# Optimization experiments

Hardware: AMD Instinct MI355X
Metric: run time of the kernel (lower is better)

Reference implementation:

```python
import jax, jax.numpy as jnp
import numpy as np

DIM, HEADS, RANK = 768, 12, 64
HEAD_DIM = DIM // HEADS

def _xavier(key, shape):
    fan_in, fan_out = shape[1], shape[0]
    std = (2.0 / (fan_in + fan_out)) ** 0.5
    return std * jax.random.normal(key, shape, dtype=jnp.float32)

def setup_inputs() -> dict:
    key = jax.random.key(0)
    ks = jax.random.split(key, 12)
    B, N = 8, 1024
    x = jax.random.normal(ks[0], (B, N, DIM), dtype=jnp.float32)
    params = {}
    for i, nm in enumerate(['Q', 'K', 'V']):
        params[f'W_{nm}0'] = _xavier(ks[1 + 3 * i], (DIM, RANK))
        params[f'W_{nm}1'] = _xavier(ks[2 + 3 * i], (HEADS, RANK))
        params[f'W_{nm}2'] = _xavier(ks[3 + 3 * i], (HEAD_DIM, RANK))
    proj_w = _xavier(ks[10], (DIM, DIM))
    proj_b = jnp.zeros((DIM,), dtype=jnp.float32)
    return dict(x=x, W_Q0=params['W_Q0'], W_Q1=params['W_Q1'], W_Q2=params['W_Q2'],
                W_K0=params['W_K0'], W_K1=params['W_K1'], W_K2=params['W_K2'],
                W_V0=params['W_V0'], W_V1=params['W_V1'], W_V2=params['W_V2'],
                proj_w=proj_w, proj_b=proj_b)

def _cp_proj(xh, W2, W1, W0, B, N, H, hd):
    # xh: [B,N,H,hd]; contract head_dim with W2 and heads with W1 -> [B,N,R], then expand to dim via W0
    t = jnp.einsum('blnd,dr,nr->blr', xh, W2, W1)
    out = jnp.einsum('blr,mr->blm', t, W0)          # [B,N,dim]
    return out.reshape(B, N, H, hd).transpose(0, 2, 1, 3)  # [B,H,N,hd]

def reference(x, W_Q0, W_Q1, W_Q2, W_K0, W_K1, W_K2, W_V0, W_V1, W_V2, proj_w, proj_b):
    B, N, C = x.shape
    H = W_Q1.shape[0]
    hd = C // H
    scale = hd ** -0.5
    xh = x.reshape(B, N, H, hd)
    q = _cp_proj(xh, W_Q2, W_Q1, W_Q0, B, N, H, hd)
    k = _cp_proj(xh, W_K2, W_K1, W_K0, B, N, H, hd)
    v = _cp_proj(xh, W_V2, W_V1, W_V0, B, N, H, hd)
    attn = jax.nn.softmax(jnp.einsum('bhqd,bhkd->bhqk', q, k) * scale, axis=-1)
    out = jnp.einsum('bhqk,bhkd->bhqd', attn, v).transpose(0, 2, 1, 3).reshape(B, N, C)
    return out @ proj_w.T + proj_b
```

## Files before the change

kernel.cpp:

```cpp
#include <hip/hip_runtime.h>

typedef unsigned short u16;
typedef __attribute__((ext_vector_type(8))) short bf16x8;
typedef __attribute__((ext_vector_type(4))) float f32x4;
typedef __attribute__((ext_vector_type(4))) unsigned short u16x4;
typedef __attribute__((ext_vector_type(8))) unsigned short u16x8;

#define AS1 __attribute__((address_space(1)))
#define AS3 __attribute__((address_space(3)))

__device__ __forceinline__ float b2f(u16 s) {
    return __uint_as_float(((unsigned)s) << 16);
}
__device__ __forceinline__ u16 f2b(float f) {
    unsigned u = __float_as_uint(f);
    unsigned r = 0x7fffu + ((u >> 16) & 1u);
    return (u16)((u + r) >> 16);
}

__device__ __forceinline__ unsigned packtrunc(float p0, float p1) {
#if __has_builtin(__builtin_amdgcn_perm)
    return __builtin_amdgcn_perm(__float_as_uint(p1), __float_as_uint(p0), 0x07060302u);
#else
    return (__float_as_uint(p0) >> 16) | (__float_as_uint(p1) & 0xffff0000u);
#endif
}

__device__ __forceinline__ void g2l16(const u16* g, u16* l) {
    __builtin_amdgcn_global_load_lds((const AS1 void*)g, (AS3 void*)l, 16, 0, 0);
}

#if __has_builtin(__builtin_amdgcn_exp2f)
#define EXP2(x) __builtin_amdgcn_exp2f(x)
#else
#define EXP2(x) exp2f(x)
#endif

__global__ __launch_bounds__(256) void build_prep(
    const float* __restrict__ Wq0, const float* __restrict__ Wq1, const float* __restrict__ Wq2,
    const float* __restrict__ Wk0, const float* __restrict__ Wk1, const float* __restrict__ Wk2,
    const float* __restrict__ Wv0, const float* __restrict__ Wv1, const float* __restrict__ Wv2,
    const float* __restrict__ PW,
    u16* __restrict__ G, u16* __restrict__ MqkT, u16* __restrict__ Dcat)
{
    const int bx = blockIdx.x;
    const int t = threadIdx.x;
    if (bx < 576) {
        const int idx = bx * 256 + t;
        const int row = idx / 768, c = idx - row * 768;
        const int which = row >> 6, r = row & 63;
        const int h = c >> 6, d = c & 63;
        const float* W1 = (which == 0) ? Wq1 : (which == 1) ? Wk1 : Wv1;
        const float* W2 = (which == 0) ? Wq2 : (which == 1) ? Wk2 : Wv2;
        G[idx] = f2b(W1[h * 64 + r] * W2[d * 64 + r]);
    } else if (bx < 624) {
        __shared__ float wq[64 * 65];
        __shared__ float wk[64 * 65];
        const int hq = bx - 576;
        const int h = hq >> 2, quarter = hq & 3;
        const float qs = 0.125f * 1.4426950408889634f;
        for (int i = t; i < 4096; i += 256) {
            const int dd = i >> 6, r = i & 63;
            wq[dd * 65 + r] = Wq0[(h * 64 + dd) * 64 + r] * qs;
            wk[dd * 65 + r] = Wk0[(h * 64 + dd) * 64 + r];
        }
        __syncthreads();
        const int j0 = quarter * 1024 + t * 4;
        const int r2 = j0 >> 6, r1b = j0 & 63;
        u16x4 pk;
#pragma unroll
        for (int jj = 0; jj < 4; ++jj) {
            float acc = 0.f;
#pragma unroll
            for (int dd = 0; dd < 64; ++dd)
                acc += wk[dd * 65 + r2] * wq[dd * 65 + r1b + jj];
            ((u16*)&pk)[jj] = f2b(acc);
        }
        *(u16x4*)(MqkT + (size_t)(h * 64 + r2) * 64 + r1b) = pk;
    } else {
        __shared__ float w0s[64 * 65];
        __shared__ float pws[32 * 65];
        const int hb = bx - 624;
        const int h = hb / 24, mBase = (hb - h * 24) * 32;
        for (int i = t; i < 4096; i += 256) {
            const int d = i >> 6, r = i & 63;
            w0s[d * 65 + r] = Wv0[(h * 64 + d) * 64 + r];
        }
        for (int i = t; i < 2048; i += 256) {
            const int mi = i >> 6, d = i & 63;
            pws[mi * 65 + d] = PW[(size_t)(mBase + mi) * 768 + h * 64 + d];
        }
        __syncthreads();
        const int r = t & 63, mi0 = t >> 6;
        float w0c[64];
#pragma unroll
        for (int d = 0; d < 64; ++d) w0c[d] = w0s[d * 65 + r];
        for (int mi = mi0; mi < 32; mi += 4) {
            float acc = 0.f;
#pragma unroll
            for (int d = 0; d < 64; ++d) acc += pws[mi * 65 + d] * w0c[d];
            Dcat[(size_t)(mBase + mi) * 768 + h * 64 + r] = f2b(acc);
        }
    }
}

__global__ __launch_bounds__(256, 2) void gemm_t(
    const float* __restrict__ X, const u16* __restrict__ G,
    u16* __restrict__ T, u16* __restrict__ tvt)
{
    __shared__ u16 As[64 * 32];
    __shared__ u16 Bs[64 * 32];

    const int tid = threadIdx.x;
    const int lane = tid & 63, wv = tid >> 6;
    const int l15 = lane & 15, quad = lane >> 4;

    const int lin = blockIdx.x + 3 * blockIdx.y;
    const int xcd = lin & 7, j = lin >> 3;
    const int col = j % 3, rowhi = j / 3;
    const int rowBase = (rowhi * 8 + xcd) * 64;
    const int colBase = col * 64;

    const int srow = tid >> 2;
    const int scol = (tid & 3) * 8;
    const float* aS = X + (size_t)(rowBase + srow) * 768 + scol;
    const u16*  bS  = G + (size_t)(colBase + srow) * 768 + scol;

    float4 a0 = *(const float4*)(aS);
    float4 a1 = *(const float4*)(aS + 4);
    int4   b0 = *(const int4*)(bS);

    const f32x4 zero4 = {0.f, 0.f, 0.f, 0.f};
    f32x4 acc[4];
#pragma unroll
    for (int tn = 0; tn < 4; ++tn) acc[tn] = zero4;

    for (int kk = 0; kk < 768; kk += 32) {
        __syncthreads();
        u16x8 ap;
        ap[0] = f2b(a0.x); ap[1] = f2b(a0.y); ap[2] = f2b(a0.z); ap[3] = f2b(a0.w);
        ap[4] = f2b(a1.x); ap[5] = f2b(a1.y); ap[6] = f2b(a1.z); ap[7] = f2b(a1.w);
        *(u16x8*)&As[srow * 32 + scol] = ap;
        *(int4*)&Bs[srow * 32 + scol]  = b0;
        __syncthreads();

        if (kk < 736) {
            a0 = *(const float4*)(aS + kk + 32);
            a1 = *(const float4*)(aS + kk + 36);
            b0 = *(const int4*)(bS + kk + 32);
        }

        const bf16x8 af = *(const bf16x8*)(As + (wv * 16 + l15) * 32 + quad * 8);
#pragma unroll
        for (int tn = 0; tn < 4; ++tn) {
            const bf16x8 bf = *(const bf16x8*)(Bs + (tn * 16 + l15) * 32 + quad * 8);
            acc[tn] = __builtin_amdgcn_mfma_f32_16x16x32_bf16(af, bf, acc[tn], 0, 0, 0);
        }
    }

    if (colBase < 128) {
#pragma unroll
        for (int tn = 0; tn < 4; ++tn) {
            const int c = colBase + tn * 16 + l15;
#pragma unroll
            for (int r = 0; r < 4; ++r) {
                const int grow = rowBase + wv * 16 + quad * 4 + r;
                T[(size_t)grow * 128 + c] = f2b(acc[tn][r]);
            }
        }
    } else {
#pragma unroll
        for (int tn = 0; tn < 4; ++tn) {
            const int rr = tn * 16 + l15;
            const int grow = rowBase + wv * 16 + quad * 4;
            u16x4 pk;
            pk.x = f2b(acc[tn][0]); pk.y = f2b(acc[tn][1]);
            pk.z = f2b(acc[tn][2]); pk.w = f2b(acc[tn][3]);
            *(u16x4*)(tvt + (size_t)rr * 8192 + grow) = pk;
        }
    }
}

__global__ __launch_bounds__(256, 3) void flash_attn10(
    const u16* __restrict__ T, const u16* __restrict__ MqkT,
    const u16* __restrict__ tvt, u16* __restrict__ Z)
{
    const int bh = blockIdx.x;
    const int qt = blockIdx.y;
    const int b = bh / 12, h = bh - b * 12;
    const u16* qp = T + ((size_t)b * 1024 + qt * 128) * 128;
    const u16* kp = T + (size_t)b * 1024 * 128 + 64;
    const u16* vp = tvt + b * 1024;

    __shared__ u16 B0raw[2 * 64 * 72];
    __shared__ u16 B1raw[2 * 64 * 72];

    const int t = threadIdx.x;
    const int lane = t & 63, wv = t >> 6;
    const int l15 = lane & 15, quad = lane >> 4;

    bf16x8 qf[2][2];
#pragma unroll
    for (int qg = 0; qg < 2; ++qg) {
        const u16* qrow = qp + (size_t)(wv * 32 + qg * 16 + l15) * 128;
        qf[qg][0] = *(const bf16x8*)(qrow + quad * 8);
        qf[qg][1] = *(const bf16x8*)(qrow + 32 + quad * 8);
    }

    const int srow = t >> 2;
    const int scol = (t & 3) * 16;
    const int p5 = srow & 31;
    const int lrow = (srow & 32) | ((p5 & 4) << 2) | ((p5 & 16) >> 1)
                   | ((p5 & 8) >> 1) | (p5 & 3);

    bf16x8 vone = {};
    if (l15 == 0) {
#pragma unroll
        for (int j = 0; j < 8; ++j) vone[j] = (short)0x3F80;
    }

    int4 kr0 = *(const int4*)(kp + (size_t)srow * 128 + scol);
    int4 kr1 = *(const int4*)(kp + (size_t)srow * 128 + scol + 8);
    int4 vr0 = *(const int4*)(vp + (size_t)srow * 8192 + scol);
    int4 vr1 = *(const int4*)(vp + (size_t)srow * 8192 + scol + 8);

    const f32x4 zero4 = {0.f, 0.f, 0.f, 0.f};
    {
        f32x4 Wt[2][4];
#pragma unroll
        for (int qg = 0; qg < 2; ++qg)
#pragma unroll
            for (int tn = 0; tn < 4; ++tn) Wt[qg][tn] = zero4;
#pragma unroll
        for (int ks = 0; ks < 2; ++ks) {
#pragma unroll
            for (int tn = 0; tn < 4; ++tn) {
                const bf16x8 mb = *(const bf16x8*)(
                    MqkT + (size_t)(h * 64 + tn * 16 + l15) * 64 + ks * 32 + quad * 8);
                Wt[0][tn] = __builtin_amdgcn_mfma_f32_16x16x32_bf16(qf[0][ks], mb, Wt[0][tn], 0, 0, 0);
                Wt[1][tn] = __builtin_amdgcn_mfma_f32_16x16x32_bf16(qf[1][ks], mb, Wt[1][tn], 0, 0, 0);
            }
        }
#pragma unroll
        for (int qg = 0; qg < 2; ++qg)
#pragma unroll
            for (int tn = 0; tn < 4; ++tn)
#pragma unroll
                for (int r = 0; r < 4; ++r)
                    B1raw[(wv * 32 + qg * 16 + quad * 4 + r) * 72 + tn * 16 + l15] =
                        f2b(Wt[qg][tn][r]);
    }
    __syncthreads();
    bf16x8 wf[2][2];
#pragma unroll
    for (int qg = 0; qg < 2; ++qg) {
        wf[qg][0] = *(const bf16x8*)&B1raw[(wv * 32 + qg * 16 + l15) * 72 + quad * 8];
        wf[qg][1] = *(const bf16x8*)&B1raw[(wv * 32 + qg * 16 + l15) * 72 + 32 + quad * 8];
    }

    *(int4*)&B0raw[lrow * 72 + scol]                 = kr0;
    *(int4*)&B0raw[lrow * 72 + scol + 8]             = kr1;
    *(int4*)&B0raw[64 * 72 + srow * 72 + scol]       = vr0;
    *(int4*)&B0raw[64 * 72 + srow * 72 + scol + 8]   = vr1;
    kr0 = *(const int4*)(kp + (size_t)(64 + srow) * 128 + scol);
    kr1 = *(const int4*)(kp + (size_t)(64 + srow) * 128 + scol + 8);
    vr0 = *(const int4*)(vp + (size_t)srow * 8192 + 64 + scol);
    vr1 = *(const int4*)(vp + (size_t)srow * 8192 + 64 + scol + 8);
    __syncthreads();

    f32x4 o_acc[2][4];
    f32x4 Lacc[2] = {zero4, zero4};
#pragma unroll
    for (int qg = 0; qg < 2; ++qg)
#pragma unroll
        for (int tn = 0; tn < 4; ++tn) o_acc[qg][tn] = zero4;

#define STAGE(NB)                                                               \
    {                                                                           \
        *(int4*)&NB[lrow * 72 + scol]               = kr0;                      \
        *(int4*)&NB[lrow * 72 + scol + 8]           = kr1;                      \
        *(int4*)&NB[64 * 72 + srow * 72 + scol]     = vr0;                      \
        *(int4*)&NB[64 * 72 + srow * 72 + scol + 8] = vr1;                      \
    }
#define PREFETCH(KT)                                                            \
    {                                                                           \
        kr0 = *(const int4*)(kp + (size_t)((KT) * 64 + srow) * 128 + scol);     \
        kr1 = *(const int4*)(kp + (size_t)((KT) * 64 + srow) * 128 + scol + 8); \
        vr0 = *(const int4*)(vp + (size_t)srow * 8192 + (KT) * 64 + scol);      \
        vr1 = *(const int4*)(vp + (size_t)srow * 8192 + (KT) * 64 + scol + 8);  \
    }
#define FLASH_TILE(KB)                                                          \
    {                                                                           \
        f32x4 Sacc[2][4];                                                       \
        _Pragma("unroll")                                                       \
        for (int qg = 0; qg < 2; ++qg)                                          \
            _Pragma("unroll")                                                   \
            for (int tk = 0; tk < 4; ++tk) Sacc[qg][tk] = zero4;                \
        _Pragma("unroll")                                                       \
        for (int ks = 0; ks < 2; ++ks) {                                        \
            _Pragma("unroll")                                                   \
            for (int tk = 0; tk < 4; ++tk) {                                    \
                const bf16x8 kf = *(const bf16x8*)&KB[(tk * 16 + l15) * 72 + ks * 32 + quad * 8]; \
                Sacc[0][tk] = __builtin_amdgcn_mfma_f32_16x16x32_bf16(kf, wf[0][ks], Sacc[0][tk], 0, 0, 0); \
                Sacc[1][tk] = __builtin_amdgcn_mfma_f32_16x16x32_bf16(kf, wf[1][ks], Sacc[1][tk], 0, 0, 0); \
            }                                                                   \
        }                                                                       \
        union { bf16x8 v; unsigned u[4]; } pf[2][2];                            \
        _Pragma("unroll")                                                       \
        for (int qg = 0; qg < 2; ++qg)                                          \
            _Pragma("unroll")                                                   \
            for (int tk = 0; tk < 4; ++tk) {                                    \
                const float p0 = EXP2(Sacc[qg][tk][0]);                         \
                const float p1 = EXP2(Sacc[qg][tk][1]);                         \
                const float p2 = EXP2(Sacc[qg][tk][2]);                         \
                const float p3 = EXP2(Sacc[qg][tk][3]);                         \
                const int g = tk >> 1, hf = (tk & 1) * 2;                       \
                pf[qg][g].u[hf + 0] = packtrunc(p0, p1);                        \
                pf[qg][g].u[hf + 1] = packtrunc(p2, p3);                        \
            }                                                                   \
        _Pragma("unroll")                                                       \
        for (int g = 0; g < 2; ++g) {                                           \
            _Pragma("unroll")                                                   \
            for (int tn = 0; tn < 4; ++tn) {                                    \
                const bf16x8 vf = *(const bf16x8*)&KB[64 * 72 + (tn * 16 + l15) * 72 + g * 32 + quad * 8]; \
                o_acc[0][tn] = __builtin_amdgcn_mfma_f32_16x16x32_bf16(pf[0][g].v, vf, o_acc[0][tn], 0, 0, 0); \
                o_acc[1][tn] = __builtin_amdgcn_mfma_f32_16x16x32_bf16(pf[1][g].v, vf, o_acc[1][tn], 0, 0, 0); \
            }                                                                   \
            Lacc[0] = __builtin_amdgcn_mfma_f32_16x16x32_bf16(pf[0][g].v, vone, Lacc[0], 0, 0, 0); \
            Lacc[1] = __builtin_amdgcn_mfma_f32_16x16x32_bf16(pf[1][g].v, vone, Lacc[1], 0, 0, 0); \
        }                                                                       \
    }

    for (int t8 = 0; t8 < 8; ++t8) {
        const int kt0 = 2 * t8;
        STAGE(B1raw);
        if (t8 < 7) PREFETCH(kt0 + 2);
        FLASH_TILE(B0raw);
        __syncthreads();
        if (t8 < 7) {
            STAGE(B0raw);
            PREFETCH(kt0 + 3);
        }
        FLASH_TILE(B1raw);
        if (t8 < 7) __syncthreads();
    }

#undef STAGE
#undef PREFETCH
#undef FLASH_TILE

#pragma unroll
    for (int qg = 0; qg < 2; ++qg) {
#pragma unroll
        for (int r = 0; r < 4; ++r) {
            const float Lv = __shfl(Lacc[qg][r], quad << 4, 64);
            const float inv = 1.0f / Lv;
            const int token = qt * 128 + wv * 32 + qg * 16 + quad * 4 + r;
#pragma unroll
            for (int tn = 0; tn < 4; ++tn) {
                const int col = h * 64 + tn * 16 + l15;
                Z[(size_t)(b * 1024 + token) * 768 + col] = f2b(o_acc[qg][tn][r] * inv);
            }
        }
    }
}

__global__ __launch_bounds__(256, 3) void gemm_out(
    const u16* __restrict__ A, const u16* __restrict__ Bt,
    float* __restrict__ C, const float* __restrict__ bias)
{
    __shared__ u16 As[128 * 32];
    __shared__ u16 Bs[64 * 32];

    const int tid  = threadIdx.x;
    const int lane = tid & 63, wv = tid >> 6;
    const int l15  = lane & 15, quad = lane >> 4;

    const int lin = blockIdx.x + 12 * blockIdx.y;
    const int xcd = lin & 7, j = lin >> 3;
    const int colT = j % 12, rowhi = j / 12;
    const int rowBase = (rowhi * 8 + xcd) * 128;
    const int colBase = colT * 64;

    const int srowA = wv * 32 + (lane >> 2);
    const int srowB = wv * 16 + (lane >> 2);
    const int scol  = (lane & 3) * 8;
    const u16* aSrc = A  + (size_t)(rowBase + srowA) * 768 + scol;
    const u16* bSrc = Bt + (size_t)(colBase + srowB) * 768 + scol;
    u16* aDst = As + wv * 1024;
    u16* bDst = Bs + wv * 512;

    const f32x4 zero4 = {0.f, 0.f, 0.f, 0.f};
    f32x4 acc[2][4];
#pragma unroll
    for (int tm = 0; tm < 2; ++tm)
#pragma unroll
        for (int tn = 0; tn < 4; ++tn) acc[tm][tn] = zero4;

    for (int kk = 0; kk < 768; kk += 32) {
        __syncthreads();
        g2l16(aSrc + kk,            aDst);
        g2l16(aSrc + kk + 16 * 768, aDst + 512);
        g2l16(bSrc + kk,            bDst);
        __syncthreads();

        bf16x8 af[2], bfm[4];
#pragma unroll
        for (int t = 0; t < 2; ++t)
            af[t]  = *(const bf16x8*)(As + (wv * 32 + t * 16 + l15) * 32 + quad * 8);
#pragma unroll
        for (int t = 0; t < 4; ++t)
            bfm[t] = *(const bf16x8*)(Bs + (t * 16 + l15) * 32 + quad * 8);
#pragma unroll
        for (int tm = 0; tm < 2; ++tm)
#pragma unroll
            for (int tn = 0; tn < 4; ++tn)
                acc[tm][tn] = __builtin_amdgcn_mfma_f32_16x16x32_bf16(
                    af[tm], bfm[tn], acc[tm][tn], 0, 0, 0);
    }

#pragma unroll
    for (int tm = 0; tm < 2; ++tm) {
        const int grow = rowBase + wv * 32 + tm * 16 + quad * 4;
#pragma unroll
        for (int tn = 0; tn < 4; ++tn) {
            const int gcol = colBase + tn * 16 + l15;
            const float bv = bias[gcol];
#pragma unroll
            for (int r = 0; r < 4; ++r)
                C[(size_t)(grow + r) * 768 + gcol] = acc[tm][tn][r] + bv;
        }
    }
}

extern "C" void kernel_launch(void* const* d_in, const int* in_sizes, int n_in,
                              void* d_out, int out_size, void* d_ws, size_t ws_size,
                              hipStream_t stream)
{
    const float* x      = (const float*)d_in[0];
    const float* Wq0    = (const float*)d_in[1];
    const float* Wq1    = (const float*)d_in[2];
    const float* Wq2    = (const float*)d_in[3];
    const float* Wk0    = (const float*)d_in[4];
    const float* Wk1    = (const float*)d_in[5];
    const float* Wk2    = (const float*)d_in[6];
    const float* Wv0    = (const float*)d_in[7];
    const float* Wv1    = (const float*)d_in[8];
    const float* Wv2    = (const float*)d_in[9];
    const float* proj_w = (const float*)d_in[10];
    const float* proj_b = (const float*)d_in[11];
    float* outp = (float*)d_out;

    char* ws = (char*)d_ws;
    u16* T    = (u16*)ws;
    u16* tvt  = (u16*)(ws + 2097152);
    u16* G    = (u16*)(ws + 3145728);
    u16* MqkT = (u16*)(ws + 3440640);
    u16* Dcat = (u16*)(ws + 3538944);
    u16* Zcat = (u16*)(ws + 4718592);

    build_prep<<<912, 256, 0, stream>>>(Wq0, Wq1, Wq2, Wk0, Wk1, Wk2, Wv0, Wv1, Wv2,
                                        proj_w, G, MqkT, Dcat);
    gemm_t<<<dim3(3, 128), 256, 0, stream>>>(x, G, T, tvt);
    flash_attn10<<<dim3(96, 8), 256, 0, stream>>>(T, MqkT, tvt, Zcat);
    gemm_out<<<dim3(12, 64), 256, 0, stream>>>(Zcat, Dcat, outp, proj_b);
}
```

Before: 172.2 us.

## Double query rows per attention block to reuse K/V tiles across more queries

Each flash-attention block now handles 256 query rows instead of 128 (64 per wave), halving the grid to 96x4 and halving K/V tile loads per query. The S computation is restructured to load K fragments once per tile and loop over four query groups, reusing them. This raises register pressure (launch bounds drop to 2 blocks per CU) and leaves only 384 blocks, which may underfill the GPU. An extra barrier is added before staging so the W scratch split across both buffers is not overwritten.

```diff
diff --git a/kernel.cpp b/kernel.cpp
--- a/kernel.cpp
+++ b/kernel.cpp
@@ -181,14 +181,14 @@
     }
 }
 
-__global__ __launch_bounds__(256, 3) void flash_attn10(
+__global__ __launch_bounds__(256, 2) void flash_attn11(
     const u16* __restrict__ T, const u16* __restrict__ MqkT,
     const u16* __restrict__ tvt, u16* __restrict__ Z)
 {
     const int bh = blockIdx.x;
     const int qt = blockIdx.y;
     const int b = bh / 12, h = bh - b * 12;
-    const u16* qp = T + ((size_t)b * 1024 + qt * 128) * 128;
+    const u16* qp = T + ((size_t)b * 1024 + qt * 256) * 128;
     const u16* kp = T + (size_t)b * 1024 * 128 + 64;
     const u16* vp = tvt + b * 1024;
 
@@ -199,10 +199,10 @@
     const int lane = t & 63, wv = t >> 6;
     const int l15 = lane & 15, quad = lane >> 4;
 
-    bf16x8 qf[2][2];
-#pragma unroll
-    for (int qg = 0; qg < 2; ++qg) {
-        const u16* qrow = qp + (size_t)(wv * 32 + qg * 16 + l15) * 128;
+    bf16x8 qf[4][2];
+#pragma unroll
+    for (int qg = 0; qg < 4; ++qg) {
+        const u16* qrow = qp + (size_t)(wv * 64 + qg * 16 + l15) * 128;
         qf[qg][0] = *(const bf16x8*)(qrow + quad * 8);
         qf[qg][1] = *(const bf16x8*)(qrow + 32 + quad * 8);
     }
@@ -225,10 +225,12 @@
     int4 vr1 = *(const int4*)(vp + (size_t)srow * 8192 + scol + 8);
 
     const f32x4 zero4 = {0.f, 0.f, 0.f, 0.f};
+    u16* const wsbuf = (wv < 2) ? B0raw : B1raw;
+    const int wrow = (wv & 1) * 64;
     {
-        f32x4 Wt[2][4];
-#pragma unroll
-        for (int qg = 0; qg < 2; ++qg)
+        f32x4 Wt[4][4];
+#pragma unroll
+        for (int qg = 0; qg < 4; ++qg)
 #pragma unroll
             for (int tn = 0; tn < 4; ++tn) Wt[qg][tn] = zero4;
 #pragma unroll
@@ -237,26 +239,29 @@
             for (int tn = 0; tn < 4; ++tn) {
                 const bf16x8 mb = *(const bf16x8*)(
                     MqkT + (size_t)(h * 64 + tn * 16 + l15) * 64 + ks * 32 + quad * 8);
-                Wt[0][tn] = __builtin_amdgcn_mfma_f32_16x16x32_bf16(qf[0][ks], mb, Wt[0][tn], 0, 0, 0);
-                Wt[1][tn] = __builtin_amdgcn_mfma_f32_16x16x32_bf16(qf[1][ks], mb, Wt[1][tn], 0, 0, 0);
+#pragma unroll
+                for (int qg = 0; qg < 4; ++qg)
+                    Wt[qg][tn] = __builtin_amdgcn_mfma_f32_16x16x32_bf16(
+                        qf[qg][ks], mb, Wt[qg][tn], 0, 0, 0);
             }
         }
 #pragma unroll
-        for (int qg = 0; qg < 2; ++qg)
+        for (int qg = 0; qg < 4; ++qg)
 #pragma unroll
             for (int tn = 0; tn < 4; ++tn)
 #pragma unroll
                 for (int r = 0; r < 4; ++r)
-                    B1raw[(wv * 32 + qg * 16 + quad * 4 + r) * 72 + tn * 16 + l15] =
+                    wsbuf[(wrow + qg * 16 + quad * 4 + r) * 72 + tn * 16 + l15] =
                         f2b(Wt[qg][tn][r]);
     }
     __syncthreads();
-    bf16x8 wf[2][2];
-#pragma unroll
-    for (int qg = 0; qg < 2; ++qg) {
-        wf[qg][0] = *(const bf16x8*)&B1raw[(wv * 32 + qg * 16 + l15) * 72 + quad * 8];
-        wf[qg][1] = *(const bf16x8*)&B1raw[(wv * 32 + qg * 16 + l15) * 72 + 32 + quad * 8];
-    }
+    bf16x8 wf[4][2];
+#pragma unroll
+    for (int qg = 0; qg < 4; ++qg) {
+        wf[qg][0] = *(const bf16x8*)&wsbuf[(wrow + qg * 16 + l15) * 72 + quad * 8];
+        wf[qg][1] = *(const bf16x8*)&wsbuf[(wrow + qg * 16 + l15) * 72 + 32 + quad * 8];
+    }
+    __syncthreads();
 
     *(int4*)&B0raw[lrow * 72 + scol]                 = kr0;
     *(int4*)&B0raw[lrow * 72 + scol + 8]             = kr1;
@@ -268,10 +273,10 @@
     vr1 = *(const int4*)(vp + (size_t)srow * 8192 + 64 + scol + 8);
     __syncthreads();
 
-    f32x4 o_acc[2][4];
-    f32x4 Lacc[2] = {zero4, zero4};
-#pragma unroll
-    for (int qg = 0; qg < 2; ++qg)
+    f32x4 o_acc[4][4];
+    f32x4 Lacc[4] = {zero4, zero4, zero4, zero4};
+#pragma unroll
+    for (int qg = 0; qg < 4; ++qg)
 #pragma unroll
         for (int tn = 0; tn < 4; ++tn) o_acc[qg][tn] = zero4;
 
@@ -291,43 +296,49 @@
     }
 #define FLASH_TILE(KB)                                                          \
     {                                                                           \
-        f32x4 Sacc[2][4];                                                       \
+        bf16x8 kf[2][4];                                                        \
         _Pragma("unroll")                                                       \
-        for (int qg = 0; qg < 2; ++qg)                                          \
-            _Pragma("unroll")                                                   \
-            for (int tk = 0; tk < 4; ++tk) Sacc[qg][tk] = zero4;                \
+        for (int ks = 0; ks < 2; ++ks)                                          \
+            _Pragma("unroll")                                                   \
+            for (int tk = 0; tk < 4; ++tk)                                      \
+                kf[ks][tk] = *(const bf16x8*)&KB[(tk * 16 + l15) * 72 + ks * 32 + quad * 8]; \
+        union { bf16x8 v; unsigned u[4]; } pf[4][2];                            \
         _Pragma("unroll")                                                       \
-        for (int ks = 0; ks < 2; ++ks) {                                        \
+        for (int qg = 0; qg < 4; ++qg) {                                        \
+            f32x4 Sacc[4];                                                      \
+            _Pragma("unroll")                                                   \
+            for (int tk = 0; tk < 4; ++tk) Sacc[tk] = zero4;                    \
+            _Pragma("unroll")                                                   \
+            for (int ks = 0; ks < 2; ++ks)                                      \
+                _Pragma("unroll")                                               \
+                for (int tk = 0; tk < 4; ++tk)                                  \
+                    Sacc[tk] = __builtin_amdgcn_mfma_f32_16x16x32_bf16(         \
+                        kf[ks][tk], wf[qg][ks], Sacc[tk], 0, 0, 0);             \
             _Pragma("unroll")                                                   \
             for (int tk = 0; tk < 4; ++tk) {                                    \
-                const bf16x8 kf = *(const bf16x8*)&KB[(tk * 16 + l15) * 72 + ks * 32 + quad * 8]; \
-                Sacc[0][tk] = __builtin_amdgcn_mfma_f32_16x16x32_bf16(kf, wf[0][ks], Sacc[0][tk], 0, 0, 0); \
-                Sacc[1][tk] = __builtin_amdgcn_mfma_f32_16x16x32_bf16(kf, wf[1][ks], Sacc[1][tk], 0, 0, 0); \
-            }                                                                   \
-        }                                                                       \
-        union { bf16x8 v; unsigned u[4]; } pf[2][2];                            \
-        _Pragma("unroll")                                                       \
-        for (int qg = 0; qg < 2; ++qg)                                          \
-            _Pragma("unroll")                                                   \
-            for (int tk = 0; tk < 4; ++tk) {                                    \
-                const float p0 = EXP2(Sacc[qg][tk][0]);                         \
-                const float p1 = EXP2(Sacc[qg][tk][1]);                         \
-                const float p2 = EXP2(Sacc[qg][tk][2]);                         \
-                const float p3 = EXP2(Sacc[qg][tk][3]);                         \
+                const float p0 = EXP2(Sacc[tk][0]);                             \
+                const float p1 = EXP2(Sacc[tk][1]);                             \
+                const float p2 = EXP2(Sacc[tk][2]);                             \
+                const float p3 = EXP2(Sacc[tk][3]);                             \
                 const int g = tk >> 1, hf = (tk & 1) * 2;                       \
                 pf[qg][g].u[hf + 0] = packtrunc(p0, p1);                        \
                 pf[qg][g].u[hf + 1] = packtrunc(p2, p3);                        \
             }                                                                   \
+        }                                                                       \
         _Pragma("unroll")                                                       \
         for (int g = 0; g < 2; ++g) {                                           \
             _Pragma("unroll")                                                   \
             for (int tn = 0; tn < 4; ++tn) {                                    \
                 const bf16x8 vf = *(const bf16x8*)&KB[64 * 72 + (tn * 16 + l15) * 72 + g * 32 + quad * 8]; \
-                o_acc[0][tn] = __builtin_amdgcn_mfma_f32_16x16x32_bf16(pf[0][g].v, vf, o_acc[0][tn], 0, 0, 0); \
-                o_acc[1][tn] = __builtin_amdgcn_mfma_f32_16x16x32_bf16(pf[1][g].v, vf, o_acc[1][tn], 0, 0, 0); \
+                _Pragma("unroll")                                               \
+                for (int qg = 0; qg < 4; ++qg)                                  \
+                    o_acc[qg][tn] = __builtin_amdgcn_mfma_f32_16x16x32_bf16(    \
+                        pf[qg][g].v, vf, o_acc[qg][tn], 0, 0, 0);               \
             }                                                                   \
-            Lacc[0] = __builtin_amdgcn_mfma_f32_16x16x32_bf16(pf[0][g].v, vone, Lacc[0], 0, 0, 0); \
-            Lacc[1] = __builtin_amdgcn_mfma_f32_16x16x32_bf16(pf[1][g].v, vone, Lacc[1], 0, 0, 0); \
+            _Pragma("unroll")                                                   \
+            for (int qg = 0; qg < 4; ++qg)                                      \
+                Lacc[qg] = __builtin_amdgcn_mfma_f32_16x16x32_bf16(             \
+                    pf[qg][g].v, vone, Lacc[qg], 0, 0, 0);                      \
         }                                                                       \
     }
 
@@ -350,12 +361,12 @@
 #undef FLASH_TILE
 
 #pragma unroll
-    for (int qg = 0; qg < 2; ++qg) {
+    for (int qg = 0; qg < 4; ++qg) {
 #pragma unroll
         for (int r = 0; r < 4; ++r) {
             const float Lv = __shfl(Lacc[qg][r], quad << 4, 64);
             const float inv = 1.0f / Lv;
-            const int token = qt * 128 + wv * 32 + qg * 16 + quad * 4 + r;
+            const int token = qt * 256 + wv * 64 + qg * 16 + quad * 4 + r;
 #pragma unroll
             for (int tn = 0; tn < 4; ++tn) {
                 const int col = h * 64 + tn * 16 + l15;
@@ -462,6 +473,6 @@
     build_prep<<<912, 256, 0, stream>>>(Wq0, Wq1, Wq2, Wk0, Wk1, Wk2, Wv0, Wv1, Wv2,
                                         proj_w, G, MqkT, Dcat);
     gemm_t<<<dim3(3, 128), 256, 0, stream>>>(x, G, T, tvt);
-    flash_attn10<<<dim3(96, 8), 256, 0, stream>>>(T, MqkT, tvt, Zcat);
+    flash_attn11<<<dim3(96, 4), 256, 0, stream>>>(T, MqkT, tvt, Zcat);
     gemm_out<<<dim3(12, 64), 256, 0, stream>>>(Zcat, Dcat, outp, proj_b);
 }
```

Measured after the change: 173.8 us. Within noise of the previous version (+0.9%).

## Fuse G construction into projection GEMM and merge prep kernels into one launch

Applied to the files above, without the earlier changes.

The separate G-building kernel and gemm_t launch are merged into one kernel. GEMM blocks now build the bf16 rank-1 B tiles on the fly from W1/W2 staged in shared memory, instead of reading a precomputed G from global memory. MqkT and Dcat prep blocks run in the same grid, which removes one launch and the G round trip. In exchange, every GEMM block recomputes the B tile products each k-step, and all block types share a 33 KB shared buffer, which may reduce occupancy for the GEMM path.

```diff
diff --git a/kernel.cpp b/kernel.cpp
--- a/kernel.cpp
+++ b/kernel.cpp
@@ -36,27 +36,110 @@
 #define EXP2(x) exp2f(x)
 #endif
 
-__global__ __launch_bounds__(256) void build_prep(
+__global__ __launch_bounds__(256, 2) void fused_t_prep(
+    const float* __restrict__ X,
     const float* __restrict__ Wq0, const float* __restrict__ Wq1, const float* __restrict__ Wq2,
     const float* __restrict__ Wk0, const float* __restrict__ Wk1, const float* __restrict__ Wk2,
     const float* __restrict__ Wv0, const float* __restrict__ Wv1, const float* __restrict__ Wv2,
     const float* __restrict__ PW,
-    u16* __restrict__ G, u16* __restrict__ MqkT, u16* __restrict__ Dcat)
+    u16* __restrict__ T, u16* __restrict__ tvt,
+    u16* __restrict__ MqkT, u16* __restrict__ Dcat)
 {
+    __shared__ __align__(16) char smem[33280];
     const int bx = blockIdx.x;
     const int t = threadIdx.x;
-    if (bx < 576) {
-        const int idx = bx * 256 + t;
-        const int row = idx / 768, c = idx - row * 768;
-        const int which = row >> 6, r = row & 63;
-        const int h = c >> 6, d = c & 63;
-        const float* W1 = (which == 0) ? Wq1 : (which == 1) ? Wk1 : Wv1;
-        const float* W2 = (which == 0) ? Wq2 : (which == 1) ? Wk2 : Wv2;
-        G[idx] = f2b(W1[h * 64 + r] * W2[d * 64 + r]);
-    } else if (bx < 624) {
-        __shared__ float wq[64 * 65];
-        __shared__ float wk[64 * 65];
-        const int hq = bx - 576;
+
+    if (bx < 384) {
+        u16*   As  = (u16*)smem;
+        u16*   Bs  = (u16*)(smem + 4096);
+        float* W1t = (float*)(smem + 8192);
+        float* W2t = (float*)(smem + 11264);
+
+        const int lane = t & 63, wv = t >> 6;
+        const int l15 = lane & 15, quad = lane >> 4;
+
+        const int lin = bx;
+        const int xcd = lin & 7, j = lin >> 3;
+        const int col = j % 3, rowhi = j / 3;
+        const int rowBase = (rowhi * 8 + xcd) * 64;
+        const int colBase = col * 64;
+
+        const float* W1g = (col == 0) ? Wq1 : (col == 1) ? Wk1 : Wv1;
+        const float* W2g = (col == 0) ? Wq2 : (col == 1) ? Wk2 : Wv2;
+        for (int i = t; i < 768; i += 256) W1t[i] = W1g[i];
+        for (int i = t; i < 4096; i += 256) {
+            const int d = i >> 6, r = i & 63;
+            W2t[r * 65 + d] = W2g[i];
+        }
+
+        const int srow = t >> 2;
+        const int scol = (t & 3) * 8;
+        const float* aS = X + (size_t)(rowBase + srow) * 768 + scol;
+
+        float4 a0 = *(const float4*)(aS);
+        float4 a1 = *(const float4*)(aS + 4);
+
+        const f32x4 zero4 = {0.f, 0.f, 0.f, 0.f};
+        f32x4 acc[4];
+#pragma unroll
+        for (int tn = 0; tn < 4; ++tn) acc[tn] = zero4;
+
+        for (int kk = 0; kk < 768; kk += 32) {
+            __syncthreads();
+            u16x8 ap;
+            ap[0] = f2b(a0.x); ap[1] = f2b(a0.y); ap[2] = f2b(a0.z); ap[3] = f2b(a0.w);
+            ap[4] = f2b(a1.x); ap[5] = f2b(a1.y); ap[6] = f2b(a1.z); ap[7] = f2b(a1.w);
+            *(u16x8*)&As[srow * 32 + scol] = ap;
+            {
+                const int c0 = kk + scol;
+                const int hh = c0 >> 6, dd = c0 & 63;
+                const float w1v = W1t[hh * 64 + srow];
+                u16x8 bp;
+#pragma unroll
+                for (int jj = 0; jj < 8; ++jj)
+                    bp[jj] = f2b(w1v * W2t[srow * 65 + dd + jj]);
+                *(u16x8*)&Bs[srow * 32 + scol] = bp;
+            }
+            __syncthreads();
+
+            if (kk < 736) {
+                a0 = *(const float4*)(aS + kk + 32);
+                a1 = *(const float4*)(aS + kk + 36);
+            }
+
+            const bf16x8 af = *(const bf16x8*)(As + (wv * 16 + l15) * 32 + quad * 8);
+#pragma unroll
+            for (int tn = 0; tn < 4; ++tn) {
+                const bf16x8 bf = *(const bf16x8*)(Bs + (tn * 16 + l15) * 32 + quad * 8);
+                acc[tn] = __builtin_amdgcn_mfma_f32_16x16x32_bf16(af, bf, acc[tn], 0, 0, 0);
+            }
+        }
+
+        if (colBase < 128) {
+#pragma unroll
+            for (int tn = 0; tn < 4; ++tn) {
+                const int c = colBase + tn * 16 + l15;
+#pragma unroll
+                for (int r = 0; r < 4; ++r) {
+                    const int grow = rowBase + wv * 16 + quad * 4 + r;
+                    T[(size_t)grow * 128 + c] = f2b(acc[tn][r]);
+                }
+            }
+        } else {
+#pragma unroll
+            for (int tn = 0; tn < 4; ++tn) {
+                const int rr = tn * 16 + l15;
+                const int grow = rowBase + wv * 16 + quad * 4;
+                u16x4 pk;
+                pk.x = f2b(acc[tn][0]); pk.y = f2b(acc[tn][1]);
+                pk.z = f2b(acc[tn][2]); pk.w = f2b(acc[tn][3]);
+                *(u16x4*)(tvt + (size_t)rr * 8192 + grow) = pk;
+            }
+        }
+    } else if (bx < 432) {
+        float* wq = (float*)smem;
+        float* wk = (float*)(smem + 16640);
+        const int hq = bx - 384;
         const int h = hq >> 2, quarter = hq & 3;
         const float qs = 0.125f * 1.4426950408889634f;
         for (int i = t; i < 4096; i += 256) {
@@ -78,9 +161,9 @@
         }
         *(u16x4*)(MqkT + (size_t)(h * 64 + r2) * 64 + r1b) = pk;
     } else {
-        __shared__ float w0s[64 * 65];
-        __shared__ float pws[32 * 65];
-        const int hb = bx - 624;
+        float* w0s = (float*)smem;
+        float* pws = (float*)(smem + 16640);
+        const int hb = bx - 432;
         const int h = hb / 24, mBase = (hb - h * 24) * 32;
         for (int i = t; i < 4096; i += 256) {
             const int d = i >> 6, r = i & 63;
@@ -100,83 +183,6 @@
 #pragma unroll
             for (int d = 0; d < 64; ++d) acc += pws[mi * 65 + d] * w0c[d];
             Dcat[(size_t)(mBase + mi) * 768 + h * 64 + r] = f2b(acc);
-        }
-    }
-}
-
-__global__ __launch_bounds__(256, 2) void gemm_t(
-    const float* __restrict__ X, const u16* __restrict__ G,
-    u16* __restrict__ T, u16* __restrict__ tvt)
-{
-    __shared__ u16 As[64 * 32];
-    __shared__ u16 Bs[64 * 32];
-
-    const int tid = threadIdx.x;
-    const int lane = tid & 63, wv = tid >> 6;
-    const int l15 = lane & 15, quad = lane >> 4;
-
-    const int lin = blockIdx.x + 3 * blockIdx.y;
-    const int xcd = lin & 7, j = lin >> 3;
-    const int col = j % 3, rowhi = j / 3;
-    const int rowBase = (rowhi * 8 + xcd) * 64;
-    const int colBase = col * 64;
-
-    const int srow = tid >> 2;
-    const int scol = (tid & 3) * 8;
-    const float* aS = X + (size_t)(rowBase + srow) * 768 + scol;
-    const u16*  bS  = G + (size_t)(colBase + srow) * 768 + scol;
-
-    float4 a0 = *(const float4*)(aS);
-    float4 a1 = *(const float4*)(aS + 4);
-    int4   b0 = *(const int4*)(bS);
-
-    const f32x4 zero4 = {0.f, 0.f, 0.f, 0.f};
-    f32x4 acc[4];
-#pragma unroll
-    for (int tn = 0; tn < 4; ++tn) acc[tn] = zero4;
-
-    for (int kk = 0; kk < 768; kk += 32) {
-        __syncthreads();
-        u16x8 ap;
-        ap[0] = f2b(a0.x); ap[1] = f2b(a0.y); ap[2] = f2b(a0.z); ap[3] = f2b(a0.w);
-        ap[4] = f2b(a1.x); ap[5] = f2b(a1.y); ap[6] = f2b(a1.z); ap[7] = f2b(a1.w);
-        *(u16x8*)&As[srow * 32 + scol] = ap;
-        *(int4*)&Bs[srow * 32 + scol]  = b0;
-        __syncthreads();
-
-        if (kk < 736) {
-            a0 = *(const float4*)(aS + kk + 32);
-            a1 = *(const float4*)(aS + kk + 36);
-            b0 = *(const int4*)(bS + kk + 32);
-        }
-
-        const bf16x8 af = *(const bf16x8*)(As + (wv * 16 + l15) * 32 + quad * 8);
-#pragma unroll
-        for (int tn = 0; tn < 4; ++tn) {
-            const bf16x8 bf = *(const bf16x8*)(Bs + (tn * 16 + l15) * 32 + quad * 8);
-            acc[tn] = __builtin_amdgcn_mfma_f32_16x16x32_bf16(af, bf, acc[tn], 0, 0, 0);
-        }
-    }
-
-    if (colBase < 128) {
-#pragma unroll
-        for (int tn = 0; tn < 4; ++tn) {
-            const int c = colBase + tn * 16 + l15;
-#pragma unroll
-            for (int r = 0; r < 4; ++r) {
-                const int grow = rowBase + wv * 16 + quad * 4 + r;
-                T[(size_t)grow * 128 + c] = f2b(acc[tn][r]);
-            }
-        }
-    } else {
-#pragma unroll
-        for (int tn = 0; tn < 4; ++tn) {
-            const int rr = tn * 16 + l15;
-            const int grow = rowBase + wv * 16 + quad * 4;
-            u16x4 pk;
-            pk.x = f2b(acc[tn][0]); pk.y = f2b(acc[tn][1]);
-            pk.z = f2b(acc[tn][2]); pk.w = f2b(acc[tn][3]);
-            *(u16x4*)(tvt + (size_t)rr * 8192 + grow) = pk;
         }
     }
 }
@@ -454,14 +460,13 @@
     char* ws = (char*)d_ws;
     u16* T    = (u16*)ws;
     u16* tvt  = (u16*)(ws + 2097152);
-    u16* G    = (u16*)(ws + 3145728);
     u16* MqkT = (u16*)(ws + 3440640);
     u16* Dcat = (u16*)(ws + 3538944);
     u16* Zcat = (u16*)(ws + 4718592);
 
-    build_prep<<<912, 256, 0, stream>>>(Wq0, Wq1, Wq2, Wk0, Wk1, Wk2, Wv0, Wv1, Wv2,
-                                        proj_w, G, MqkT, Dcat);
-    gemm_t<<<dim3(3, 128), 256, 0, stream>>>(x, G, T, tvt);
+    fused_t_prep<<<720, 256, 0, stream>>>(x, Wq0, Wq1, Wq2, Wk0, Wk1, Wk2,
+                                          Wv0, Wv1, Wv2, proj_w,
+                                          T, tvt, MqkT, Dcat);
     flash_attn10<<<dim3(96, 8), 256, 0, stream>>>(T, MqkT, tvt, Zcat);
     gemm_out<<<dim3(12, 64), 256, 0, stream>>>(Zcat, Dcat, outp, proj_b);
 }
```

Measured after the change: 163.1 us. -5.3%, faster.
